# Performance work log

Measured on AMD Instinct MI355X. Metric: run time of the kernel, lower is better.

The kernel has to match this reference:

```python
import jax, jax.numpy as jnp
import numpy as np

EPS = 1e-8  # torch F.cosine_similarity eps


def setup_inputs() -> dict:
    key = jax.random.key(0)
    tensor = jax.random.normal(key, (8192, 256), dtype=jnp.float32)
    return {"tensor": tensor}


def reference(tensor):
    # cosine similarity: L2-normalize rows (norm clamped to eps, matching torch), then Gram GEMM
    norms = jnp.linalg.norm(tensor, axis=-1, keepdims=True)  # [N,1]
    x_hat = tensor / jnp.maximum(norms, EPS)                  # [N,D]
    sim = x_hat @ x_hat.T                                     # [N,N] cosine similarity
    # row-normalize adjacency
    row_sum = jnp.sum(sim, axis=1, keepdims=True)             # [N,1]
    adj = sim / row_sum                                       # [N,N]
    # aggregate
    return adj @ tensor                                       # [N,D]
```

## Files before the change

### kernel.cpp

```cpp
#include <hip/hip_runtime.h>

#define N_ROWS 8192
#define DIM 256
#define EPSF 1e-8f

typedef _Float16 f16x8 __attribute__((ext_vector_type(8)));
typedef float f32x4 __attribute__((ext_vector_type(4)));

__global__ __launch_bounds__(256) void k1_norm(const float* __restrict__ T,
                                               float* __restrict__ inv_norm,
                                               double* __restrict__ s) {
    __shared__ double sacc[4][DIM];
    const int tid = threadIdx.x, bid = blockIdx.x;
    const int lane = tid & 63, wave = tid >> 6;
    double a0 = 0, a1 = 0, a2 = 0, a3 = 0;
#pragma unroll
    for (int r = 0; r < 4; ++r) {
        int row = bid * 16 + wave * 4 + r;
        float4 v = ((const float4*)(T + (size_t)row * DIM))[lane];
        float ss = v.x * v.x + v.y * v.y + v.z * v.z + v.w * v.w;
#pragma unroll
        for (int o = 32; o; o >>= 1) ss += __shfl_down(ss, o);
        ss = __shfl(ss, 0);
        float inv = 1.0f / fmaxf(sqrtf(ss), EPSF);
        if (lane == 0) inv_norm[row] = inv;
        a0 += (double)(v.x * inv);
        a1 += (double)(v.y * inv);
        a2 += (double)(v.z * inv);
        a3 += (double)(v.w * inv);
    }
    sacc[wave][lane * 4 + 0] = a0;
    sacc[wave][lane * 4 + 1] = a1;
    sacc[wave][lane * 4 + 2] = a2;
    sacc[wave][lane * 4 + 3] = a3;
    __syncthreads();
    double t = sacc[0][tid] + sacc[1][tid] + sacc[2][tid] + sacc[3][tid];
    atomicAdd(&s[tid], t);
}

__global__ __launch_bounds__(256) void k2_gemm_rs(const float* __restrict__ T,
                                                  const float* __restrict__ inv_norm,
                                                  const double* __restrict__ s,
                                                  float* __restrict__ inv_rs,
                                                  float* __restrict__ partials) {
    __shared__ _Float16 As[2][64][40];
    __shared__ _Float16 Bs[2][64][40];
    const int tid = threadIdx.x, bid = blockIdx.x;
    const int lane = tid & 63, wave = tid >> 6;

    if (bid >= 512) {
        const int row = (bid - 512) * 4 + wave;
        const double s0 = s[lane * 4 + 0];
        const double s1 = s[lane * 4 + 1];
        const double s2 = s[lane * 4 + 2];
        const double s3 = s[lane * 4 + 3];
        float4 v = ((const float4*)(T + (size_t)row * DIM))[lane];
        double d = (double)v.x * s0 + (double)v.y * s1 +
                   (double)v.z * s2 + (double)v.w * s3;
#pragma unroll
        for (int o = 32; o; o >>= 1) d += __shfl_down(d, o);
        if (lane == 0)
            inv_rs[row] = (float)(1.0 / (d * (double)inv_norm[row]));
        return;
    }

    const int g = bid;
    const int k0 = (g & 3) * 64;
    const int d0 = ((g >> 2) & 3) * 64;
    const int i0 = (g >> 4) * 256;
    const int wy = wave >> 1, wx = wave & 1;
    const int lm = lane & 15, lg = lane >> 4;
    const int i = tid & 31, c8 = (tid >> 5) * 8;
    f32x4 acc[2][2] = {};
    float4 rA[2], rB[2];
    float rI;

    auto stage = [&](int ic) {
        int gi = i0 + ic + i;
        rI = inv_norm[gi];
        const float* rowp = T + (size_t)gi * DIM;
        rA[0] = *(const float4*)(rowp + k0 + c8);
        rA[1] = *(const float4*)(rowp + k0 + c8 + 4);
        rB[0] = *(const float4*)(rowp + d0 + c8);
        rB[1] = *(const float4*)(rowp + d0 + c8 + 4);
    };
    auto commit = [&](int buf) {
#pragma unroll
        for (int j = 0; j < 2; ++j) {
            float4 a = rA[j], b = rB[j];
            int c = c8 + j * 4;
            As[buf][c + 0][i] = (_Float16)(a.x * rI);
            As[buf][c + 1][i] = (_Float16)(a.y * rI);
            As[buf][c + 2][i] = (_Float16)(a.z * rI);
            As[buf][c + 3][i] = (_Float16)(a.w * rI);
            Bs[buf][c + 0][i] = (_Float16)b.x;
            Bs[buf][c + 1][i] = (_Float16)b.y;
            Bs[buf][c + 2][i] = (_Float16)b.z;
            Bs[buf][c + 3][i] = (_Float16)b.w;
        }
    };
    auto compute = [&](int buf) {
        f16x8 af[2], bf[2];
#pragma unroll
        for (int mt = 0; mt < 2; ++mt)
            af[mt] = *(const f16x8*)&As[buf][wy * 32 + mt * 16 + lm][lg * 8];
#pragma unroll
        for (int nt = 0; nt < 2; ++nt)
            bf[nt] = *(const f16x8*)&Bs[buf][wx * 32 + nt * 16 + lm][lg * 8];
#pragma unroll
        for (int mt = 0; mt < 2; ++mt)
#pragma unroll
            for (int nt = 0; nt < 2; ++nt)
                acc[mt][nt] = __builtin_amdgcn_mfma_f32_16x16x32_f16(
                    af[mt], bf[nt], acc[mt][nt], 0, 0, 0);
    };

    stage(0);
    commit(0);
    __syncthreads();
    for (int c = 1; c < 8; ++c) {
        stage(c * 32);
        compute((c - 1) & 1);
        commit(c & 1);
        __syncthreads();
    }
    compute(1);

    float* pz = partials + (size_t)(g >> 4) * 65536;
#pragma unroll
    for (int mt = 0; mt < 2; ++mt) {
        int km = k0 + wy * 32 + mt * 16 + lg * 4;
#pragma unroll
        for (int nt = 0; nt < 2; ++nt) {
            int dn = d0 + wx * 32 + nt * 16 + lm;
#pragma unroll
            for (int r = 0; r < 4; ++r)
                pz[(size_t)(km + r) * 256 + dn] = acc[mt][nt][r];
        }
    }
}

__global__ __launch_bounds__(256) void k_reduceM(const float* __restrict__ partials,
                                                 _Float16* __restrict__ Mt) {
    const int gidx = blockIdx.x * 256 + threadIdx.x;
    const int k = gidx >> 8, d = gidx & 255;
    const float* p = partials + (size_t)k * 256 + d;
    float a0 = 0.f, a1 = 0.f, a2 = 0.f, a3 = 0.f;
#pragma unroll
    for (int z = 0; z < 32; z += 4) {
        a0 += p[(size_t)(z + 0) * 65536];
        a1 += p[(size_t)(z + 1) * 65536];
        a2 += p[(size_t)(z + 2) * 65536];
        a3 += p[(size_t)(z + 3) * 65536];
    }
    Mt[(size_t)d * 256 + k] = (_Float16)((a0 + a1) + (a2 + a3));
}

__global__ __launch_bounds__(256) void k3_mfma(const float* __restrict__ T,
                                               const float* __restrict__ inv_norm,
                                               const _Float16* __restrict__ Mt,
                                               const float* __restrict__ inv_rs,
                                               float* __restrict__ out) {
    __shared__ _Float16 As[2][32][40];
    __shared__ _Float16 Bs[2][64][40];
    const int tid = threadIdx.x, bid = blockIdx.x;
    const int lane = tid & 63, wave = tid >> 6;
    const int i0 = (bid >> 2) * 32;
    const int d0 = (bid & 3) * 64;
    const int wy = wave >> 1, wx = wave & 1;
    const int lm = lane & 15, lg = lane >> 4;
    f32x4 acc[2] = {};
    float4 rA;
    float rI;
    f16x8 rB;
    const int ia = tid >> 3, c4 = (tid & 7) * 4;
    const int db = tid >> 2, k8 = (tid & 3) * 8;

    auto stage = [&](int kc) {
        rI = inv_norm[i0 + ia];
        rA = *(const float4*)(T + (size_t)(i0 + ia) * DIM + kc + c4);
        rB = *(const f16x8*)(Mt + (size_t)(d0 + db) * 256 + kc + k8);
    };
    auto commit = [&](int buf) {
        As[buf][ia][c4 + 0] = (_Float16)(rA.x * rI);
        As[buf][ia][c4 + 1] = (_Float16)(rA.y * rI);
        As[buf][ia][c4 + 2] = (_Float16)(rA.z * rI);
        As[buf][ia][c4 + 3] = (_Float16)(rA.w * rI);
        *(f16x8*)&Bs[buf][db][k8] = rB;
    };
    auto compute = [&](int buf) {
        f16x8 af = *(const f16x8*)&As[buf][wy * 16 + lm][lg * 8];
        f16x8 bf0 = *(const f16x8*)&Bs[buf][wx * 32 + lm][lg * 8];
        f16x8 bf1 = *(const f16x8*)&Bs[buf][wx * 32 + 16 + lm][lg * 8];
        acc[0] = __builtin_amdgcn_mfma_f32_16x16x32_f16(af, bf0, acc[0], 0, 0, 0);
        acc[1] = __builtin_amdgcn_mfma_f32_16x16x32_f16(af, bf1, acc[1], 0, 0, 0);
    };

    stage(0);
    commit(0);
    __syncthreads();
    for (int c = 1; c < 8; ++c) {
        stage(c * 32);
        compute((c - 1) & 1);
        commit(c & 1);
        __syncthreads();
    }
    compute(1);

#pragma unroll
    for (int r = 0; r < 4; ++r) {
        int gi = i0 + wy * 16 + lg * 4 + r;
        float ir = inv_rs[gi];
        out[(size_t)gi * DIM + d0 + wx * 32 + lm] = acc[0][r] * ir;
        out[(size_t)gi * DIM + d0 + wx * 32 + 16 + lm] = acc[1][r] * ir;
    }
}

extern "C" void kernel_launch(void* const* d_in, const int* in_sizes, int n_in,
                              void* d_out, int out_size, void* d_ws, size_t ws_size,
                              hipStream_t stream) {
    const float* T = (const float*)d_in[0];
    float* out = (float*)d_out;

    char* ws = (char*)d_ws;
    float* inv_norm = (float*)(ws);
    double* s = (double*)(ws + 32768);
    float* inv_rs = (float*)(ws + 34816);
    _Float16* Mt = (_Float16*)(ws + 67584);
    float* partials = (float*)(ws + 198656);

    hipMemsetAsync(s, 0, 256 * sizeof(double), stream);
    k1_norm<<<512, 256, 0, stream>>>(T, inv_norm, s);
    k2_gemm_rs<<<2560, 256, 0, stream>>>(T, inv_norm, s, inv_rs, partials);
    k_reduceM<<<256, 256, 0, stream>>>(partials, Mt);
    k3_mfma<<<1024, 256, 0, stream>>>(T, inv_norm, Mt, inv_rs, out);
}
```

Baseline: 94.78 us.

## Fuse Gram GEMM, reduction and output GEMM into one persistent kernel with counters

Merges the split-K Gram GEMM, row-sum pass, partial reduction and final aggregation GEMM into a single launch. Dependent block groups spin on global atomic counters instead of waiting at kernel boundaries. The row-sum blocks now handle 16 rows each, the reduction blocks 4 elements each, and the final GEMM tile grows to 64x64 so fewer blocks are needed. This removes two launches and their tail gaps, but it assumes blocks are scheduled in order and that producers stay resident, and the spin-waiting blocks hold CU slots while they wait.

```diff
diff --git a/kernel.cpp b/kernel.cpp
--- a/kernel.cpp
+++ b/kernel.cpp
@@ -38,181 +38,232 @@
     atomicAdd(&s[tid], t);
 }
 
-__global__ __launch_bounds__(256) void k2_gemm_rs(const float* __restrict__ T,
-                                                  const float* __restrict__ inv_norm,
-                                                  const double* __restrict__ s,
-                                                  float* __restrict__ inv_rs,
-                                                  float* __restrict__ partials) {
+__global__ __launch_bounds__(256, 7) void k2_all(
+    const float* __restrict__ T, const float* __restrict__ inv_norm,
+    const double* __restrict__ s, float* __restrict__ inv_rs,
+    float* __restrict__ partials, _Float16* __restrict__ Mt,
+    float* __restrict__ out, int* __restrict__ counters)
+{
     __shared__ _Float16 As[2][64][40];
     __shared__ _Float16 Bs[2][64][40];
     const int tid = threadIdx.x, bid = blockIdx.x;
     const int lane = tid & 63, wave = tid >> 6;
 
-    if (bid >= 512) {
-        const int row = (bid - 512) * 4 + wave;
+    if (bid < 512) {
+        const int g = bid;
+        const int k0 = (g & 3) * 64;
+        const int d0 = ((g >> 2) & 3) * 64;
+        const int i0 = (g >> 4) * 256;
+        const int wy = wave >> 1, wx = wave & 1;
+        const int lm = lane & 15, lg = lane >> 4;
+        const int i = tid & 31, c8 = (tid >> 5) * 8;
+        f32x4 acc[2][2] = {};
+        float4 rA[2], rB[2];
+        float rI;
+
+        auto stage = [&](int ic) {
+            int gi = i0 + ic + i;
+            rI = inv_norm[gi];
+            const float* rowp = T + (size_t)gi * DIM;
+            rA[0] = *(const float4*)(rowp + k0 + c8);
+            rA[1] = *(const float4*)(rowp + k0 + c8 + 4);
+            rB[0] = *(const float4*)(rowp + d0 + c8);
+            rB[1] = *(const float4*)(rowp + d0 + c8 + 4);
+        };
+        auto commit = [&](int buf) {
+#pragma unroll
+            for (int j = 0; j < 2; ++j) {
+                float4 a = rA[j], b = rB[j];
+                int c = c8 + j * 4;
+                As[buf][c + 0][i] = (_Float16)(a.x * rI);
+                As[buf][c + 1][i] = (_Float16)(a.y * rI);
+                As[buf][c + 2][i] = (_Float16)(a.z * rI);
+                As[buf][c + 3][i] = (_Float16)(a.w * rI);
+                Bs[buf][c + 0][i] = (_Float16)b.x;
+                Bs[buf][c + 1][i] = (_Float16)b.y;
+                Bs[buf][c + 2][i] = (_Float16)b.z;
+                Bs[buf][c + 3][i] = (_Float16)b.w;
+            }
+        };
+        auto compute = [&](int buf) {
+            f16x8 af[2], bf[2];
+#pragma unroll
+            for (int mt = 0; mt < 2; ++mt)
+                af[mt] = *(const f16x8*)&As[buf][wy * 32 + mt * 16 + lm][lg * 8];
+#pragma unroll
+            for (int nt = 0; nt < 2; ++nt)
+                bf[nt] = *(const f16x8*)&Bs[buf][wx * 32 + nt * 16 + lm][lg * 8];
+#pragma unroll
+            for (int mt = 0; mt < 2; ++mt)
+#pragma unroll
+                for (int nt = 0; nt < 2; ++nt)
+                    acc[mt][nt] = __builtin_amdgcn_mfma_f32_16x16x32_f16(
+                        af[mt], bf[nt], acc[mt][nt], 0, 0, 0);
+        };
+
+        stage(0);
+        commit(0);
+        __syncthreads();
+        for (int c = 1; c < 8; ++c) {
+            stage(c * 32);
+            compute((c - 1) & 1);
+            commit(c & 1);
+            __syncthreads();
+        }
+        compute(1);
+
+        float* pz = partials + (size_t)(g >> 4) * 65536;
+#pragma unroll
+        for (int mt = 0; mt < 2; ++mt) {
+            int km = k0 + wy * 32 + mt * 16 + lg * 4;
+#pragma unroll
+            for (int nt = 0; nt < 2; ++nt) {
+                int dn = d0 + wx * 32 + nt * 16 + lm;
+#pragma unroll
+                for (int r = 0; r < 4; ++r)
+                    pz[(size_t)(km + r) * 256 + dn] = acc[mt][nt][r];
+            }
+        }
+        __threadfence();
+        __syncthreads();
+        if (tid == 0) atomicAdd(&counters[0], 1);
+        return;
+    }
+
+    if (bid < 1024) {
+        const int base = (bid - 512) * 16 + wave * 4;
         const double s0 = s[lane * 4 + 0];
         const double s1 = s[lane * 4 + 1];
         const double s2 = s[lane * 4 + 2];
         const double s3 = s[lane * 4 + 3];
-        float4 v = ((const float4*)(T + (size_t)row * DIM))[lane];
-        double d = (double)v.x * s0 + (double)v.y * s1 +
-                   (double)v.z * s2 + (double)v.w * s3;
-#pragma unroll
-        for (int o = 32; o; o >>= 1) d += __shfl_down(d, o);
-        if (lane == 0)
-            inv_rs[row] = (float)(1.0 / (d * (double)inv_norm[row]));
+#pragma unroll
+        for (int r = 0; r < 4; ++r) {
+            int row = base + r;
+            float4 v = ((const float4*)(T + (size_t)row * DIM))[lane];
+            double d = (double)v.x * s0 + (double)v.y * s1 +
+                       (double)v.z * s2 + (double)v.w * s3;
+#pragma unroll
+            for (int o = 32; o; o >>= 1) d += __shfl_down(d, o);
+            if (lane == 0)
+                inv_rs[row] = (float)(1.0 / (d * (double)inv_norm[row]));
+        }
+        __threadfence();
+        __syncthreads();
+        if (tid == 0) atomicAdd(&counters[1], 1);
         return;
     }
 
-    const int g = bid;
-    const int k0 = (g & 3) * 64;
-    const int d0 = ((g >> 2) & 3) * 64;
-    const int i0 = (g >> 4) * 256;
-    const int wy = wave >> 1, wx = wave & 1;
-    const int lm = lane & 15, lg = lane >> 4;
-    const int i = tid & 31, c8 = (tid >> 5) * 8;
-    f32x4 acc[2][2] = {};
-    float4 rA[2], rB[2];
-    float rI;
-
-    auto stage = [&](int ic) {
-        int gi = i0 + ic + i;
-        rI = inv_norm[gi];
-        const float* rowp = T + (size_t)gi * DIM;
-        rA[0] = *(const float4*)(rowp + k0 + c8);
-        rA[1] = *(const float4*)(rowp + k0 + c8 + 4);
-        rB[0] = *(const float4*)(rowp + d0 + c8);
-        rB[1] = *(const float4*)(rowp + d0 + c8 + 4);
-    };
-    auto commit = [&](int buf) {
-#pragma unroll
-        for (int j = 0; j < 2; ++j) {
-            float4 a = rA[j], b = rB[j];
-            int c = c8 + j * 4;
-            As[buf][c + 0][i] = (_Float16)(a.x * rI);
-            As[buf][c + 1][i] = (_Float16)(a.y * rI);
-            As[buf][c + 2][i] = (_Float16)(a.z * rI);
-            As[buf][c + 3][i] = (_Float16)(a.w * rI);
-            Bs[buf][c + 0][i] = (_Float16)b.x;
-            Bs[buf][c + 1][i] = (_Float16)b.y;
-            Bs[buf][c + 2][i] = (_Float16)b.z;
-            Bs[buf][c + 3][i] = (_Float16)b.w;
-        }
-    };
-    auto compute = [&](int buf) {
-        f16x8 af[2], bf[2];
-#pragma unroll
-        for (int mt = 0; mt < 2; ++mt)
-            af[mt] = *(const f16x8*)&As[buf][wy * 32 + mt * 16 + lm][lg * 8];
-#pragma unroll
-        for (int nt = 0; nt < 2; ++nt)
-            bf[nt] = *(const f16x8*)&Bs[buf][wx * 32 + nt * 16 + lm][lg * 8];
-#pragma unroll
-        for (int mt = 0; mt < 2; ++mt)
-#pragma unroll
-            for (int nt = 0; nt < 2; ++nt)
-                acc[mt][nt] = __builtin_amdgcn_mfma_f32_16x16x32_f16(
-                    af[mt], bf[nt], acc[mt][nt], 0, 0, 0);
-    };
-
-    stage(0);
-    commit(0);
-    __syncthreads();
-    for (int c = 1; c < 8; ++c) {
-        stage(c * 32);
-        compute((c - 1) & 1);
-        commit(c & 1);
-        __syncthreads();
-    }
-    compute(1);
-
-    float* pz = partials + (size_t)(g >> 4) * 65536;
-#pragma unroll
-    for (int mt = 0; mt < 2; ++mt) {
-        int km = k0 + wy * 32 + mt * 16 + lg * 4;
-#pragma unroll
-        for (int nt = 0; nt < 2; ++nt) {
-            int dn = d0 + wx * 32 + nt * 16 + lm;
-#pragma unroll
-            for (int r = 0; r < 4; ++r)
-                pz[(size_t)(km + r) * 256 + dn] = acc[mt][nt][r];
-        }
-    }
-}
-
-__global__ __launch_bounds__(256) void k_reduceM(const float* __restrict__ partials,
-                                                 _Float16* __restrict__ Mt) {
-    const int gidx = blockIdx.x * 256 + threadIdx.x;
-    const int k = gidx >> 8, d = gidx & 255;
-    const float* p = partials + (size_t)k * 256 + d;
-    float a0 = 0.f, a1 = 0.f, a2 = 0.f, a3 = 0.f;
-#pragma unroll
-    for (int z = 0; z < 32; z += 4) {
-        a0 += p[(size_t)(z + 0) * 65536];
-        a1 += p[(size_t)(z + 1) * 65536];
-        a2 += p[(size_t)(z + 2) * 65536];
-        a3 += p[(size_t)(z + 3) * 65536];
-    }
-    Mt[(size_t)d * 256 + k] = (_Float16)((a0 + a1) + (a2 + a3));
-}
-
-__global__ __launch_bounds__(256) void k3_mfma(const float* __restrict__ T,
-                                               const float* __restrict__ inv_norm,
-                                               const _Float16* __restrict__ Mt,
-                                               const float* __restrict__ inv_rs,
-                                               float* __restrict__ out) {
-    __shared__ _Float16 As[2][32][40];
-    __shared__ _Float16 Bs[2][64][40];
-    const int tid = threadIdx.x, bid = blockIdx.x;
-    const int lane = tid & 63, wave = tid >> 6;
-    const int i0 = (bid >> 2) * 32;
-    const int d0 = (bid & 3) * 64;
-    const int wy = wave >> 1, wx = wave & 1;
-    const int lm = lane & 15, lg = lane >> 4;
-    f32x4 acc[2] = {};
-    float4 rA;
-    float rI;
-    f16x8 rB;
-    const int ia = tid >> 3, c4 = (tid & 7) * 4;
-    const int db = tid >> 2, k8 = (tid & 3) * 8;
-
-    auto stage = [&](int kc) {
-        rI = inv_norm[i0 + ia];
-        rA = *(const float4*)(T + (size_t)(i0 + ia) * DIM + kc + c4);
-        rB = *(const f16x8*)(Mt + (size_t)(d0 + db) * 256 + kc + k8);
-    };
-    auto commit = [&](int buf) {
-        As[buf][ia][c4 + 0] = (_Float16)(rA.x * rI);
-        As[buf][ia][c4 + 1] = (_Float16)(rA.y * rI);
-        As[buf][ia][c4 + 2] = (_Float16)(rA.z * rI);
-        As[buf][ia][c4 + 3] = (_Float16)(rA.w * rI);
-        *(f16x8*)&Bs[buf][db][k8] = rB;
-    };
-    auto compute = [&](int buf) {
-        f16x8 af = *(const f16x8*)&As[buf][wy * 16 + lm][lg * 8];
-        f16x8 bf0 = *(const f16x8*)&Bs[buf][wx * 32 + lm][lg * 8];
-        f16x8 bf1 = *(const f16x8*)&Bs[buf][wx * 32 + 16 + lm][lg * 8];
-        acc[0] = __builtin_amdgcn_mfma_f32_16x16x32_f16(af, bf0, acc[0], 0, 0, 0);
-        acc[1] = __builtin_amdgcn_mfma_f32_16x16x32_f16(af, bf1, acc[1], 0, 0, 0);
-    };
-
-    stage(0);
-    commit(0);
-    __syncthreads();
-    for (int c = 1; c < 8; ++c) {
-        stage(c * 32);
-        compute((c - 1) & 1);
-        commit(c & 1);
-        __syncthreads();
-    }
-    compute(1);
-
-#pragma unroll
-    for (int r = 0; r < 4; ++r) {
-        int gi = i0 + wy * 16 + lg * 4 + r;
-        float ir = inv_rs[gi];
-        out[(size_t)gi * DIM + d0 + wx * 32 + lm] = acc[0][r] * ir;
-        out[(size_t)gi * DIM + d0 + wx * 32 + 16 + lm] = acc[1][r] * ir;
+    if (bid < 1088) {
+        if (tid == 0)
+            while (atomicAdd(&counters[0], 0) < 512) __builtin_amdgcn_s_sleep(8);
+        __syncthreads();
+        __threadfence();
+        const int b = bid - 1024;
+#pragma unroll
+        for (int q = 0; q < 4; ++q) {
+            int g = b * 1024 + q * 256 + tid;
+            int k = g >> 8, d = g & 255;
+            const float* p = partials + (size_t)k * 256 + d;
+            float a0 = 0.f, a1 = 0.f, a2 = 0.f, a3 = 0.f;
+#pragma unroll
+            for (int z = 0; z < 32; z += 4) {
+                a0 += p[(size_t)(z + 0) * 65536];
+                a1 += p[(size_t)(z + 1) * 65536];
+                a2 += p[(size_t)(z + 2) * 65536];
+                a3 += p[(size_t)(z + 3) * 65536];
+            }
+            Mt[(size_t)d * 256 + k] = (_Float16)((a0 + a1) + (a2 + a3));
+        }
+        __threadfence();
+        __syncthreads();
+        if (tid == 0) atomicAdd(&counters[2], 1);
+        return;
+    }
+
+    {
+        if (tid == 0) {
+            while (atomicAdd(&counters[2], 0) < 64) __builtin_amdgcn_s_sleep(8);
+            while (atomicAdd(&counters[1], 0) < 512) __builtin_amdgcn_s_sleep(8);
+        }
+        __syncthreads();
+        __threadfence();
+
+        const int t = bid - 1088;
+        const int i0 = (t >> 2) * 64;
+        const int d0 = (t & 3) * 64;
+        const int wy = wave >> 1, wx = wave & 1;
+        const int lm = lane & 15, lg = lane >> 4;
+        f32x4 acc[2][2] = {};
+        float4 rA[2];
+        float rI[2];
+        f16x8 rB;
+        const int db = tid >> 2, k8 = (tid & 3) * 8;
+
+        auto stage = [&](int kc) {
+#pragma unroll
+            for (int j = 0; j < 2; ++j) {
+                int idx = tid + 256 * j;
+                int ia = idx >> 3;
+                int c4 = (idx & 7) * 4;
+                int gi = i0 + ia;
+                rI[j] = inv_norm[gi];
+                rA[j] = *(const float4*)(T + (size_t)gi * DIM + kc + c4);
+            }
+            rB = *(const f16x8*)(Mt + (size_t)(d0 + db) * 256 + kc + k8);
+        };
+        auto commit = [&](int buf) {
+#pragma unroll
+            for (int j = 0; j < 2; ++j) {
+                int idx = tid + 256 * j;
+                int ia = idx >> 3;
+                int c4 = (idx & 7) * 4;
+                float inv = rI[j];
+                As[buf][ia][c4 + 0] = (_Float16)(rA[j].x * inv);
+                As[buf][ia][c4 + 1] = (_Float16)(rA[j].y * inv);
+                As[buf][ia][c4 + 2] = (_Float16)(rA[j].z * inv);
+                As[buf][ia][c4 + 3] = (_Float16)(rA[j].w * inv);
+            }
+            *(f16x8*)&Bs[buf][db][k8] = rB;
+        };
+        auto compute = [&](int buf) {
+            f16x8 af[2], bf[2];
+#pragma unroll
+            for (int ti = 0; ti < 2; ++ti)
+                af[ti] = *(const f16x8*)&As[buf][wy * 32 + ti * 16 + lm][lg * 8];
+#pragma unroll
+            for (int tj = 0; tj < 2; ++tj)
+                bf[tj] = *(const f16x8*)&Bs[buf][wx * 32 + tj * 16 + lm][lg * 8];
+#pragma unroll
+            for (int ti = 0; ti < 2; ++ti)
+#pragma unroll
+                for (int tj = 0; tj < 2; ++tj)
+                    acc[ti][tj] = __builtin_amdgcn_mfma_f32_16x16x32_f16(
+                        af[ti], bf[tj], acc[ti][tj], 0, 0, 0);
+        };
+
+        stage(0);
+        commit(0);
+        __syncthreads();
+        for (int c = 1; c < 8; ++c) {
+            stage(c * 32);
+            compute((c - 1) & 1);
+            commit(c & 1);
+            __syncthreads();
+        }
+        compute(1);
+
+#pragma unroll
+        for (int ti = 0; ti < 2; ++ti) {
+#pragma unroll
+            for (int r = 0; r < 4; ++r) {
+                int gi = i0 + wy * 32 + ti * 16 + lg * 4 + r;
+                float ir = inv_rs[gi];
+#pragma unroll
+                for (int tj = 0; tj < 2; ++tj)
+                    out[(size_t)gi * DIM + d0 + wx * 32 + tj * 16 + lm] =
+                        acc[ti][tj][r] * ir;
+            }
+        }
     }
 }
 
@@ -225,13 +276,13 @@
     char* ws = (char*)d_ws;
     float* inv_norm = (float*)(ws);
     double* s = (double*)(ws + 32768);
-    float* inv_rs = (float*)(ws + 34816);
-    _Float16* Mt = (_Float16*)(ws + 67584);
-    float* partials = (float*)(ws + 198656);
-
-    hipMemsetAsync(s, 0, 256 * sizeof(double), stream);
+    int* counters = (int*)(ws + 34816);
+    float* inv_rs = (float*)(ws + 34880);
+    _Float16* Mt = (_Float16*)(ws + 67648);
+    float* partials = (float*)(ws + 198720);
+
+    hipMemsetAsync(ws + 32768, 0, 2112, stream);
     k1_norm<<<512, 256, 0, stream>>>(T, inv_norm, s);
-    k2_gemm_rs<<<2560, 256, 0, stream>>>(T, inv_norm, s, inv_rs, partials);
-    k_reduceM<<<256, 256, 0, stream>>>(partials, Mt);
-    k3_mfma<<<1024, 256, 0, stream>>>(T, inv_norm, Mt, inv_rs, out);
+    k2_all<<<1600, 256, 0, stream>>>(T, inv_norm, s, inv_rs, partials, Mt,
+                                     out, counters);
 }
```

Result: slower. 317.9 us (+235.4%).

## Replace split-K partial buffer with float atomics and fuse row-sum into final GEMM

Applied to the files above, without the earlier changes.

The Gram-matrix kernel now accumulates its split-K contributions straight into an fp32 transposed M with atomicAdd, so the separate reduction kernel and the 8 MB partials buffer go away. The row-sum reciprocal computation moves from extra blocks of the GEMM kernel into the final GEMM kernel, where each block computes its 32 rows into shared memory. The final kernel now reads fp32 M and converts it to fp16 itself. This removes one launch and a large write/read round trip, at the cost of atomic contention (32-way per element), non-deterministic summation order, and redundant row-sum work repeated across the 4 column blocks that share each row group.

```diff
diff --git a/kernel.cpp b/kernel.cpp
--- a/kernel.cpp
+++ b/kernel.cpp
@@ -38,31 +38,13 @@
     atomicAdd(&s[tid], t);
 }
 
-__global__ __launch_bounds__(256) void k2_gemm_rs(const float* __restrict__ T,
-                                                  const float* __restrict__ inv_norm,
-                                                  const double* __restrict__ s,
-                                                  float* __restrict__ inv_rs,
-                                                  float* __restrict__ partials) {
+__global__ __launch_bounds__(256) void k2_gemmM(const float* __restrict__ T,
+                                                const float* __restrict__ inv_norm,
+                                                float* __restrict__ Mt) {
     __shared__ _Float16 As[2][64][40];
     __shared__ _Float16 Bs[2][64][40];
     const int tid = threadIdx.x, bid = blockIdx.x;
     const int lane = tid & 63, wave = tid >> 6;
-
-    if (bid >= 512) {
-        const int row = (bid - 512) * 4 + wave;
-        const double s0 = s[lane * 4 + 0];
-        const double s1 = s[lane * 4 + 1];
-        const double s2 = s[lane * 4 + 2];
-        const double s3 = s[lane * 4 + 3];
-        float4 v = ((const float4*)(T + (size_t)row * DIM))[lane];
-        double d = (double)v.x * s0 + (double)v.y * s1 +
-                   (double)v.z * s2 + (double)v.w * s3;
-#pragma unroll
-        for (int o = 32; o; o >>= 1) d += __shfl_down(d, o);
-        if (lane == 0)
-            inv_rs[row] = (float)(1.0 / (d * (double)inv_norm[row]));
-        return;
-    }
 
     const int g = bid;
     const int k0 = (g & 3) * 64;
@@ -126,7 +108,6 @@
     }
     compute(1);
 
-    float* pz = partials + (size_t)(g >> 4) * 65536;
 #pragma unroll
     for (int mt = 0; mt < 2; ++mt) {
         int km = k0 + wy * 32 + mt * 16 + lg * 4;
@@ -135,34 +116,19 @@
             int dn = d0 + wx * 32 + nt * 16 + lm;
 #pragma unroll
             for (int r = 0; r < 4; ++r)
-                pz[(size_t)(km + r) * 256 + dn] = acc[mt][nt][r];
+                atomicAdd(&Mt[(size_t)dn * 256 + km + r], acc[mt][nt][r]);
         }
     }
-}
-
-__global__ __launch_bounds__(256) void k_reduceM(const float* __restrict__ partials,
-                                                 _Float16* __restrict__ Mt) {
-    const int gidx = blockIdx.x * 256 + threadIdx.x;
-    const int k = gidx >> 8, d = gidx & 255;
-    const float* p = partials + (size_t)k * 256 + d;
-    float a0 = 0.f, a1 = 0.f, a2 = 0.f, a3 = 0.f;
-#pragma unroll
-    for (int z = 0; z < 32; z += 4) {
-        a0 += p[(size_t)(z + 0) * 65536];
-        a1 += p[(size_t)(z + 1) * 65536];
-        a2 += p[(size_t)(z + 2) * 65536];
-        a3 += p[(size_t)(z + 3) * 65536];
-    }
-    Mt[(size_t)d * 256 + k] = (_Float16)((a0 + a1) + (a2 + a3));
 }
 
 __global__ __launch_bounds__(256) void k3_mfma(const float* __restrict__ T,
                                                const float* __restrict__ inv_norm,
-                                               const _Float16* __restrict__ Mt,
-                                               const float* __restrict__ inv_rs,
+                                               const float* __restrict__ Mt,
+                                               const double* __restrict__ s,
                                                float* __restrict__ out) {
     __shared__ _Float16 As[2][32][40];
     __shared__ _Float16 Bs[2][64][40];
+    __shared__ float irs[32];
     const int tid = threadIdx.x, bid = blockIdx.x;
     const int lane = tid & 63, wave = tid >> 6;
     const int i0 = (bid >> 2) * 32;
@@ -172,21 +138,28 @@
     f32x4 acc[2] = {};
     float4 rA;
     float rI;
-    f16x8 rB;
+    float4 rBf[2];
     const int ia = tid >> 3, c4 = (tid & 7) * 4;
     const int db = tid >> 2, k8 = (tid & 3) * 8;
 
     auto stage = [&](int kc) {
         rI = inv_norm[i0 + ia];
         rA = *(const float4*)(T + (size_t)(i0 + ia) * DIM + kc + c4);
-        rB = *(const f16x8*)(Mt + (size_t)(d0 + db) * 256 + kc + k8);
+        const float* mp = Mt + (size_t)(d0 + db) * 256 + kc + k8;
+        rBf[0] = *(const float4*)(mp);
+        rBf[1] = *(const float4*)(mp + 4);
     };
     auto commit = [&](int buf) {
         As[buf][ia][c4 + 0] = (_Float16)(rA.x * rI);
         As[buf][ia][c4 + 1] = (_Float16)(rA.y * rI);
         As[buf][ia][c4 + 2] = (_Float16)(rA.z * rI);
         As[buf][ia][c4 + 3] = (_Float16)(rA.w * rI);
-        *(f16x8*)&Bs[buf][db][k8] = rB;
+        f16x8 h;
+        h[0] = (_Float16)rBf[0].x; h[1] = (_Float16)rBf[0].y;
+        h[2] = (_Float16)rBf[0].z; h[3] = (_Float16)rBf[0].w;
+        h[4] = (_Float16)rBf[1].x; h[5] = (_Float16)rBf[1].y;
+        h[6] = (_Float16)rBf[1].z; h[7] = (_Float16)rBf[1].w;
+        *(f16x8*)&Bs[buf][db][k8] = h;
     };
     auto compute = [&](int buf) {
         f16x8 af = *(const f16x8*)&As[buf][wy * 16 + lm][lg * 8];
@@ -197,6 +170,23 @@
     };
 
     stage(0);
+    {
+        const double s0 = s[lane * 4 + 0];
+        const double s1 = s[lane * 4 + 1];
+        const double s2 = s[lane * 4 + 2];
+        const double s3 = s[lane * 4 + 3];
+#pragma unroll
+        for (int rr = 0; rr < 8; ++rr) {
+            int row = i0 + wave * 8 + rr;
+            float4 v = ((const float4*)(T + (size_t)row * DIM))[lane];
+            double d = (double)v.x * s0 + (double)v.y * s1 +
+                       (double)v.z * s2 + (double)v.w * s3;
+#pragma unroll
+            for (int o = 32; o; o >>= 1) d += __shfl_down(d, o);
+            if (lane == 0)
+                irs[wave * 8 + rr] = (float)(1.0 / (d * (double)inv_norm[row]));
+        }
+    }
     commit(0);
     __syncthreads();
     for (int c = 1; c < 8; ++c) {
@@ -209,8 +199,9 @@
 
 #pragma unroll
     for (int r = 0; r < 4; ++r) {
-        int gi = i0 + wy * 16 + lg * 4 + r;
-        float ir = inv_rs[gi];
+        int li = wy * 16 + lg * 4 + r;
+        int gi = i0 + li;
+        float ir = irs[li];
         out[(size_t)gi * DIM + d0 + wx * 32 + lm] = acc[0][r] * ir;
         out[(size_t)gi * DIM + d0 + wx * 32 + 16 + lm] = acc[1][r] * ir;
     }
@@ -225,13 +216,10 @@
     char* ws = (char*)d_ws;
     float* inv_norm = (float*)(ws);
     double* s = (double*)(ws + 32768);
-    float* inv_rs = (float*)(ws + 34816);
-    _Float16* Mt = (_Float16*)(ws + 67584);
-    float* partials = (float*)(ws + 198656);
-
-    hipMemsetAsync(s, 0, 256 * sizeof(double), stream);
+    float* Mt = (float*)(ws + 34816);
+
+    hipMemsetAsync(ws + 32768, 0, 264192, stream);
     k1_norm<<<512, 256, 0, stream>>>(T, inv_norm, s);
-    k2_gemm_rs<<<2560, 256, 0, stream>>>(T, inv_norm, s, inv_rs, partials);
-    k_reduceM<<<256, 256, 0, stream>>>(partials, Mt);
-    k3_mfma<<<1024, 256, 0, stream>>>(T, inv_norm, Mt, inv_rs, out);
-}
+    k2_gemmM<<<512, 256, 0, stream>>>(T, inv_norm, Mt);
+    k3_mfma<<<1024, 256, 0, stream>>>(T, inv_norm, Mt, s, out);
+}
```

New measurement: 126.4 us. 33.3% more time.
